# Kernel tuning notes

Hardware: AMD Instinct MI355X
Metric: run time of the kernel (lower is better)

The kernel has to match this reference:

```python
import jax, jax.numpy as jnp
import numpy as np


def conv2d(x, w, pad):
    # x: [N,C,H,W], w: [O,I,kh,kw]
    return jax.lax.conv_general_dilated(
        x, w, window_strides=(1, 1), padding=[(pad, pad), (pad, pad)],
        dimension_numbers=("NCHW", "OIHW", "NCHW"))


def group_norm1(x, g, b, eps=1e-5):
    # GroupNorm(1, C): normalize over (C,H,W) per sample, per-channel affine
    mu = jnp.mean(x, axis=(1, 2, 3), keepdims=True)
    var = jnp.mean((x - mu) ** 2, axis=(1, 2, 3), keepdims=True)
    xn = (x - mu) * jax.lax.rsqrt(var + eps)
    return xn * g[None, :, None, None] + b[None, :, None, None]


def maxpool_3x3_s2(x):
    return jax.lax.reduce_window(
        x, -jnp.inf, jax.lax.max, (1, 1, 3, 3), (1, 1, 2, 2),
        ((0, 0), (0, 0), (1, 1), (1, 1)))


def hr2o_layer(x, wq, wk, wv, wo, g, b):
    # x: [N,C,H,W]; pairwise attention over the N ROIs at each (h,w)
    q = conv2d(x, wq, 1)
    k = conv2d(x, wk, 1)
    v = conv2d(x, wv, 1)
    scale = 1.0 / jnp.sqrt(jnp.asarray(x.shape[1], x.dtype))
    # torch: (q.unsqueeze(1) * k.unsqueeze(0)).sum(2) == einsum over channels
    att = jnp.einsum("nchw,mchw->nmhw", q, k) * scale  # [N,N,H,W]
    att = jax.nn.softmax(att, axis=1)                    # softmax over keys (dim=1)
    virt = jnp.einsum("nmhw,mchw->nchw", att, v)        # [N,C,H,W]
    virt = jax.nn.relu(group_norm1(virt, g, b))
    virt = conv2d(virt, wo, 1)
    return x + virt  # dropout is identity in eval mode


def setup_inputs() -> dict:
    key = jax.random.key(0)
    ks = jax.random.split(key, 12)
    N, C_R, H, W, HID, NCLS, DEPTH = 64, 1024, 16, 16, 512, 60, 2
    s = 0.02
    return {
        "bg_feats": jax.random.normal(ks[0], (C_R, H, W), jnp.float32),
        "actor_feats": jax.random.normal(ks[1], (N, C_R), jnp.float32),
        "w_conv1": jax.random.normal(ks[2], (HID, 2 * C_R, 1, 1), jnp.float32) * s,
        "w_conv2": jax.random.normal(ks[3], (HID, HID, 3, 3), jnp.float32) * s,
        "w_q": jax.random.normal(ks[4], (DEPTH, HID, HID, 3, 3), jnp.float32) * s,
        "w_k": jax.random.normal(ks[5], (DEPTH, HID, HID, 3, 3), jnp.float32) * s,
        "w_v": jax.random.normal(ks[6], (DEPTH, HID, HID, 3, 3), jnp.float32) * s,
        "w_o": jax.random.normal(ks[7], (DEPTH, HID, HID, 3, 3), jnp.float32) * s,
        "gamma": jnp.ones((DEPTH, HID), jnp.float32),
        "beta": jnp.zeros((DEPTH, HID), jnp.float32),
        "w_fc1": jax.random.normal(ks[8], (HID, C_R), jnp.float32) * s,
        "w_fc2": jax.random.normal(ks[9], (NCLS, 2 * HID), jnp.float32) * s,
    }


def reference(bg_feats, actor_feats, w_conv1, w_conv2, w_q, w_k, w_v, w_o,
              gamma, beta, w_fc1, w_fc2):
    N = actor_feats.shape[0]
    C_R, H, W = bg_feats.shape
    # bg repeated per ROI, actor features tiled over spatial dims
    bg = jnp.broadcast_to(bg_feats[None], (N, C_R, H, W))
    tiled = jnp.broadcast_to(actor_feats[:, :, None, None], (N, C_R, H, W))
    x = jnp.concatenate([bg, tiled], axis=1)           # [N, 2*C_R, H, W]
    x = jax.nn.relu(conv2d(x, w_conv1, 0))             # 1x1 -> [N,HID,H,W]
    x = jax.nn.relu(conv2d(x, w_conv2, 0))             # 3x3 pad=0 -> H-2,W-2
    x = maxpool_3x3_s2(x)                              # -> 7x7
    for d in range(w_q.shape[0]):
        x = hr2o_layer(x, w_q[d], w_k[d], w_v[d], w_o[d], gamma[d], beta[d])
    high_order = jnp.mean(x, axis=(2, 3))              # gap -> [N,HID]
    roi = jax.nn.relu(actor_feats @ w_fc1.T)           # [N,HID]
    out = jnp.concatenate([roi, high_order], axis=1) @ w_fc2.T  # [N,num_classes]
    return out
```

## Files before the change

### kernel.cpp

```cpp
#include <hip/hip_runtime.h>
#include <math.h>


typedef __bf16 bf16x8 __attribute__((ext_vector_type(8)));
typedef float  f32x4  __attribute__((ext_vector_type(4)));

#define NROI 64
#define CR   1024
#define HIDC 512
#define NCLS 60
#define PLANE (NROI * HIDC * 49)
#define ROWH 40
#define OCALL 4608
#define TAPSTR ((size_t)OCALL * 512)
#define WL (HIDC * HIDC * 9)
#define GNCNT 25088.0f

#if defined(__has_builtin)
#  if __has_builtin(__builtin_amdgcn_global_load_lds)
#    define HAVE_GLL 1
#  endif
#endif

__device__ __forceinline__ void stage16(const void* g, void* lds_base, int lane) {
#ifdef HAVE_GLL
    __builtin_amdgcn_global_load_lds(
        (const __attribute__((address_space(1))) unsigned int*)g,
        (__attribute__((address_space(3))) unsigned int*)lds_base, 16, 0, 0);
#else
    *(uint4*)((char*)lds_base + lane * 16) = *(const uint4*)g;
#endif
}

__device__ __forceinline__ float bf2f(unsigned short h) {
    union { unsigned u; float f; } x; x.u = (unsigned)h << 16; return x.f;
}

__global__ __launch_bounds__(256) void k_misc(
    const float* __restrict__ w2, const float* __restrict__ wq,
    const float* __restrict__ wk, const float* __restrict__ wv,
    const float* __restrict__ wo, const float* __restrict__ bg,
    __bf16* __restrict__ wAll, __bf16* __restrict__ inT7,
    __bf16* __restrict__ bgT)
{
    const int b = blockIdx.x, tid = threadIdx.x;
    if (b < 4608) {
        const int bid = b;
        const float* src;
        if (bid < 512) src = w2 + (size_t)bid * 4608;
        else if (bid < 2048) {
            const int r = bid - 512;
            const float* bb = r < 512 ? wq : (r < 1024 ? wk : wv);
            src = bb + (size_t)(r & 511) * 4608;
        } else if (bid < 2560) src = wo + (size_t)(bid - 2048) * 4608;
        else if (bid < 4096) {
            const int r = bid - 2560;
            const float* bb = r < 512 ? wq : (r < 1024 ? wk : wv);
            src = bb + WL + (size_t)(r & 511) * 4608;
        } else src = wo + WL + (size_t)(bid - 4096) * 4608;
        __shared__ float s[4608];
        const float4* s4 = (const float4*)src;
        for (int i = tid; i < 1152; i += 256) ((float4*)s)[i] = s4[i];
        __syncthreads();
        unsigned* dst = (unsigned*)wAll;
        const int c = tid * 2;
        const int swz = ((c >> 3) & 3) ^ ((bid >> 1) & 3);
        const size_t cidx = (size_t)(c >> 5) * 32 + swz * 8 + (c & 7);
#pragma unroll
        for (int t = 0; t < 9; ++t) {
            const unsigned short u0 = __builtin_bit_cast(unsigned short, (__bf16)s[c * 9 + t]);
            const unsigned short u1 = __builtin_bit_cast(unsigned short, (__bf16)s[(c + 1) * 9 + t]);
            dst[((size_t)t * TAPSTR + (size_t)bid * 512 + cidx) / 2] =
                ((unsigned)u1 << 16) | u0;
        }
    } else if (b < 5120) {
        const int k = b - 4608;
        const int n = k >> 3;
        const int j0 = (k & 7) * 4;
#pragma unroll
        for (int i = 0; i < 4; ++i) {
            const int jj = j0 + i;
            int sp;
            if (jj < 9) sp = jj;
            else if (jj < 18) sp = 63 + jj;
            else { const int t = jj - 18; sp = (1 + (t >> 1)) * 9 + (t & 1) * 8; }
            unsigned* d = (unsigned*)(inT7 + ((size_t)n * 81 + sp) * 512);
            d[tid] = 0u;
        }
    } else {
        const int cb = (b - 5120) * 8;
        const int p = tid;
        bf16x8 v;
#pragma unroll
        for (int j = 0; j < 8; ++j)
            v[j] = (__bf16)bg[(size_t)(cb + j) * 256 + p];
        *(bf16x8*)(bgT + (size_t)p * 1024 + cb) = v;
    }
}

__global__ __launch_bounds__(256, 2) void k_ab(
    const __bf16* __restrict__ bgT, const float* __restrict__ actor,
    const float* __restrict__ w1, const float* __restrict__ wfc1,
    float* __restrict__ A_T, float* __restrict__ Bp, float* __restrict__ roi)
{
    const int bx = blockIdx.x, by = blockIdx.y;
    const bool isA = bx < 4;
    const bool isRoi = (bx == 5);
    const int ocWg = by * 64;
    const int tid = threadIdx.x;
    const int w = tid >> 6, lane = tid & 63;
    const int q = lane >> 4, l16 = lane & 15;

    __shared__ __align__(16) __bf16 s_a[64 * ROWH];
    __shared__ __align__(16) __bf16 s_b[64 * ROWH];

    f32x4 acc[4];
#pragma unroll
    for (int nt = 0; nt < 4; ++nt) acc[nt] = (f32x4){0.f, 0.f, 0.f, 0.f};

    const int row = tid >> 2, part = tid & 3;
    for (int ch = 0; ch < 32; ++ch) {
        const int c0 = ch * 32;
        __syncthreads();
        if (isA) {
            const uint4 vv = *(const uint4*)(
                bgT + (size_t)(bx * 64 + row) * 1024 + c0 + part * 8);
            *(uint4*)(&s_a[row * ROWH + part * 8]) = vv;
        } else {
            const float* src = actor + (size_t)row * CR + c0 + part * 8;
            bf16x8 val;
#pragma unroll
            for (int j = 0; j < 8; ++j) val[j] = (__bf16)src[j];
            *(bf16x8*)(&s_a[row * ROWH + part * 8]) = val;
        }
        {
            const float* srcb = isRoi
                ? (wfc1 + (size_t)(ocWg + row) * CR + c0 + part * 8)
                : (w1 + (size_t)(ocWg + row) * (2 * CR)
                      + (isA ? 0 : CR) + c0 + part * 8);
            bf16x8 vb;
#pragma unroll
            for (int j = 0; j < 8; ++j) vb[j] = (__bf16)srcb[j];
            *(bf16x8*)(&s_b[row * ROWH + part * 8]) = vb;
        }
        __syncthreads();
        const bf16x8 af = *(const bf16x8*)(&s_a[(w * 16 + l16) * ROWH + q * 8]);
#pragma unroll
        for (int nt = 0; nt < 4; ++nt) {
            const bf16x8 bw = *(const bf16x8*)(&s_b[(nt * 16 + l16) * ROWH + q * 8]);
            acc[nt] = __builtin_amdgcn_mfma_f32_16x16x32_bf16(af, bw, acc[nt], 0, 0, 0);
        }
    }
#pragma unroll
    for (int r = 0; r < 4; ++r) {
#pragma unroll
        for (int nt = 0; nt < 4; ++nt) {
            const int mrow = w * 16 + q * 4 + r;
            const int oc = ocWg + nt * 16 + l16;
            if (isA)       A_T[(size_t)(bx * 64 + mrow) * 512 + oc] = acc[nt][r];
            else if (isRoi) roi[(size_t)mrow * 512 + oc] = fmaxf(acc[nt][r], 0.f);
            else           Bp[(size_t)mrow * 512 + oc] = acc[nt][r];
        }
    }
}

__global__ __launch_bounds__(256) void k_prep_in2(
    const float* __restrict__ A_T, const float* __restrict__ B,
    __bf16* __restrict__ dst)
{
    const int vn = blockIdx.x;
    const int n = vn >> 2, quad = vn & 3;
    const int sp0 = blockIdx.y * 27;
    const float b0 = B[n * HIDC + threadIdx.x];
    const float b1 = B[n * HIDC + 256 + threadIdx.x];
    for (int sp = sp0; sp < sp0 + 27; ++sp) {
        const int r = sp / 9, w = sp % 9;
        const int p16 = ((quad >> 1) * 7 + r) * 16 + (quad & 1) * 7 + w;
        __bf16* d = dst + ((size_t)vn * 81 + sp) * 512;
        d[threadIdx.x]       = (__bf16)fmaxf(A_T[p16 * HIDC + threadIdx.x] + b0, 0.f);
        d[256 + threadIdx.x] = (__bf16)fmaxf(A_T[p16 * HIDC + 256 + threadIdx.x] + b1, 0.f);
    }
}

__global__ __launch_bounds__(256) void k_prep_gn(
    const float* __restrict__ virt, const float* __restrict__ statsRaw,
    const float* __restrict__ gamma, const float* __restrict__ beta,
    __bf16* __restrict__ gnT)
{
    const int vn = blockIdx.x;
    const int sp0 = blockIdx.y * 9;
    __shared__ float s_mi[2];
    if (threadIdx.x == 0) {
        const float S = statsRaw[vn * 2], Q = statsRaw[vn * 2 + 1];
        const float mean = S / GNCNT;
        s_mi[0] = mean;
        s_mi[1] = rsqrtf(Q / GNCNT - mean * mean + 1e-5f);
    }
    __syncthreads();
    const float m = s_mi[0], iv = s_mi[1];
    const int c0 = threadIdx.x, c1 = threadIdx.x + 256;
    const float g0 = gamma[c0], g1 = gamma[c1];
    const float b0 = beta[c0],  b1 = beta[c1];
    for (int sp = sp0; sp < sp0 + 9; ++sp) {
        const int rr = sp / 9, cc = sp % 9;
        __bf16* d = gnT + ((size_t)vn * 81 + sp) * 512;
        if (rr >= 1 && rr <= 7 && cc >= 1 && cc <= 7) {
            const int p = (rr - 1) * 7 + (cc - 1);
            const float* src = virt + ((size_t)vn * 49 + p) * 512;
            d[c0] = (__bf16)fmaxf((src[c0] - m) * iv * g0 + b0, 0.f);
            d[c1] = (__bf16)fmaxf((src[c1] - m) * iv * g1 + b1, 0.f);
        } else {
            d[c0] = (__bf16)0.f;
            d[c1] = (__bf16)0.f;
        }
    }
}

template<int VN, int MODE>
__global__ __launch_bounds__(256, (VN == 4) ? 2 : 3) void k_conv_pipe(
    const __bf16* __restrict__ inT,
    const __bf16* __restrict__ wAll, int ocBaseGl,
    __bf16* __restrict__ outb,
    float* __restrict__ zeroStats, float* __restrict__ gapZero,
    const float* __restrict__ resid, float* __restrict__ outf,
    __bf16* __restrict__ inT7out, float* __restrict__ gapOut)
{
    constexpr int MT = (VN == 4) ? 4 : 2;
    constexpr int SLOTS = VN * 324;
    constexpr int NSUB = (SLOTS + 255) / 256;
    constexpr int SBUF = NSUB * 256;
    constexpr int NI = NSUB / 3;
    const int tid = threadIdx.x;
    const int w = tid >> 6, lane = tid & 63;
    const int q = lane >> 4, l16 = lane & 15;
    const int vn_l = (VN == 4) ? w : (w & 1);
    const int mh   = (VN == 4) ? 0 : (w >> 1);
    const int vnBase = blockIdx.x * VN;
    const int ocWg = blockIdx.y * 64;

    if (zeroStats && blockIdx.x == 0 && blockIdx.y == 0 && tid < 128)
        zeroStats[tid] = 0.f;
    if (gapZero && blockIdx.y == 0 && blockIdx.x < 16) {
        const float4 z = {0.f, 0.f, 0.f, 0.f};
        ((float4*)gapZero)[blockIdx.x * 512 + tid * 2]     = z;
        ((float4*)gapZero)[blockIdx.x * 512 + tid * 2 + 1] = z;
    }

    __shared__ __align__(16) __bf16 s_w[2 * 3 * 2048];
    __shared__ __align__(16) __bf16 s_in[2 * SBUF * 8];

    unsigned iGo[NSUB];
#pragma unroll
    for (int s = 0; s < NSUB; ++s) {
        int idx = tid + s * 256;
        if (idx > SLOTS - 1) idx = SLOTS - 1;
        const int vnl = idx / 324, rem = idx - vnl * 324;
        const int r = rem >> 2, part = rem & 3;
        iGo[s] = (unsigned)(((vnBase + vnl) * 81 + r) * 512
                            + ((part ^ (r & 3)) * 8));
    }
    const unsigned wGo = (unsigned)((ocBaseGl + ocWg + (tid >> 2)) * 512
                                    + (tid & 3) * 8);
    const int bOff = l16 * 32 + ((q ^ ((l16 >> 1) & 3)) << 3);

    int aLoc[MT];
#pragma unroll
    for (int mt = 0; mt < MT; ++mt) {
        int p = (mh * MT + mt) * 16 + l16;
        p = p > 48 ? 48 : p;
        aLoc[mt] = (p / 7) * 9 + (p % 7);
    }
    const int vb81 = vn_l * 81;

    f32x4 acc[MT][4];
#pragma unroll
    for (int a = 0; a < MT; ++a)
#pragma unroll
        for (int b = 0; b < 4; ++b) acc[a][b] = (f32x4){0.f, 0.f, 0.f, 0.f};

#pragma unroll
    for (int s = 0; s < NSUB; ++s)
        stage16(inT + iGo[s],
                (char*)s_in + (size_t)(s * 256 + w * 64) * 16, lane);
#pragma unroll
    for (int j = 0; j < 3; ++j)
        stage16(wAll + (size_t)j * TAPSTR + wGo,
                (char*)s_w + (size_t)j * 4096 + (size_t)w * 1024, lane);
    __syncthreads();

    for (int ch = 0; ch < 16; ++ch) {
        const int c0 = ch * 32;
        const int cur = ch & 1;
        const int nxt = cur ^ 1;
#pragma unroll
        for (int f = 0; f < 3; ++f) {
            const int P = ch * 3 + f;
            const int wpar = P & 1;
            {
                const int fn = (f == 2) ? 0 : (f + 1);
                const int cc = (f == 2) ? (c0 + 32) : c0;
#pragma unroll
                for (int j = 0; j < 3; ++j)
                    stage16(wAll + (size_t)(fn * 3 + j) * TAPSTR + wGo + cc,
                            (char*)s_w + (size_t)((wpar ^ 1) * 3 + j) * 4096
                                        + (size_t)w * 1024, lane);
            }
#pragma unroll
            for (int u = 0; u < NI; ++u) {
                const int s = f * NI + u;
                stage16(inT + iGo[s] + c0 + 32,
                        (char*)s_in + (size_t)nxt * (SBUF * 16)
                                    + (size_t)(s * 256 + w * 64) * 16, lane);
            }
            if (f == 0) {
                if constexpr (NI == 2) asm volatile("s_waitcnt vmcnt(5)" ::: "memory");
                else                   asm volatile("s_waitcnt vmcnt(4)" ::: "memory");
            } else {
                if constexpr (NI == 2) asm volatile("s_waitcnt vmcnt(7)" ::: "memory");
                else                   asm volatile("s_waitcnt vmcnt(5)" ::: "memory");
            }
            __builtin_amdgcn_sched_barrier(0);
            __builtin_amdgcn_s_barrier();
            __builtin_amdgcn_sched_barrier(0);
            __builtin_amdgcn_s_setprio(1);
#pragma unroll
            for (int j = 0; j < 3; ++j) {
                const int DT = f * 9 + j;
                bf16x8 bw[4];
#pragma unroll
                for (int nt = 0; nt < 4; ++nt)
                    bw[nt] = *(const bf16x8*)(
                        &s_w[(wpar * 3 + j) * 2048 + nt * 512 + bOff]);
                bf16x8 af[MT];
#pragma unroll
                for (int mt = 0; mt < MT; ++mt) {
                    const int rl = aLoc[mt] + DT;
                    const int col = (q ^ (rl & 3)) << 3;
                    af[mt] = *(const bf16x8*)(
                        &s_in[cur * (SBUF * 8) + (vb81 + rl) * 32 + col]);
                }
#pragma unroll
                for (int mt = 0; mt < MT; ++mt)
#pragma unroll
                    for (int nt = 0; nt < 4; ++nt)
                        acc[mt][nt] = __builtin_amdgcn_mfma_f32_16x16x32_bf16(
                            af[mt], bw[nt], acc[mt][nt], 0, 0, 0);
            }
            __builtin_amdgcn_s_setprio(0);
            __builtin_amdgcn_sched_barrier(0);
            __builtin_amdgcn_s_barrier();
        }
    }

    const int vn = vnBase + vn_l;
    float gsum[4] = {0.f, 0.f, 0.f, 0.f};
#pragma unroll
    for (int mt = 0; mt < MT; ++mt) {
#pragma unroll
        for (int r = 0; r < 4; ++r) {
            const int p = (mh * MT + mt) * 16 + q * 4 + r;
            if (p >= 49) continue;
#pragma unroll
            for (int nt = 0; nt < 4; ++nt) {
                const int oc = ocWg + nt * 16 + l16;
                const float v = acc[mt][nt][r];
                if constexpr (MODE == 2) {
                    const int n = vn >> 2, quad = vn & 3;
                    const int p14 = ((quad >> 1) * 7 + p / 7) * 14 + (quad & 1) * 7 + p % 7;
                    outb[((size_t)n * 196 + p14) * 512 + oc] = (__bf16)fmaxf(v, 0.f);
                } else if constexpr (MODE == 1) {
                    const size_t addr = ((size_t)vn * 49 + p) * 512 + oc;
                    const float res = v + resid[addr];
                    if (!gapOut) outf[addr] = res;
                    gsum[nt] += res;
                    if (inT7out) {
                        const int sp = (p / 7 + 1) * 9 + (p % 7 + 1);
                        inT7out[((size_t)vn * 81 + sp) * 512 + oc] = (__bf16)res;
                    }
                } else {
                    const int conv = oc >> 9;
                    outb[(size_t)conv * PLANE + ((size_t)p * 64 + vn) * 512 + (oc & 511)]
                        = (__bf16)v;
                }
            }
        }
    }
    if constexpr (MODE == 1) {
        if (gapOut) {
#pragma unroll
            for (int nt = 0; nt < 4; ++nt)
                atomicAdd(gapOut + (size_t)vn * 512 + ocWg + nt * 16 + l16, gsum[nt]);
        }
    }
}

__global__ __launch_bounds__(256) void k_pool_prep(
    const __bf16* __restrict__ x2, __bf16* __restrict__ inT7,
    float* __restrict__ xA)
{
    const int b = blockIdx.x;
    const int n = b / 49, p = b % 49;
    const int i = p / 7, j = p % 7;
    const int sp = (i + 1) * 9 + (j + 1);
#pragma unroll
    for (int k = 0; k < 2; ++k) {
        const int c = threadIdx.x + k * 256;
        float mx = -1e30f;
#pragma unroll
        for (int di = -1; di <= 1; ++di) {
            const int rr = 2 * i + di;
            if (rr < 0 || rr >= 14) continue;
#pragma unroll
            for (int dj = -1; dj <= 1; ++dj) {
                const int cc = 2 * j + dj;
                if (cc < 0 || cc >= 14) continue;
                mx = fmaxf(mx, (float)x2[((size_t)n * 196 + rr * 14 + cc) * 512 + c]);
            }
        }
        inT7[((size_t)n * 81 + sp) * 512 + c] = (__bf16)mx;
        xA[((size_t)n * 49 + p) * 512 + c] = mx;
    }
}

__global__ __launch_bounds__(256) void k_attvirt(
    const __bf16* __restrict__ qT, const __bf16* __restrict__ kT,
    const __bf16* __restrict__ vT, float* __restrict__ virt,
    float* __restrict__ statsRaw)
{
    const int p = blockIdx.y;
    const int w = threadIdx.x >> 6, m = threadIdx.x & 63;
    const int n = blockIdx.x * 4 + w;
    __shared__ float s_q[4][HIDC];
    __shared__ float s_a[4][64];
    {
        const uint4 v = ((const uint4*)(qT + ((size_t)p * 64 + n) * HIDC))[m];
        const unsigned* u = (const unsigned*)&v;
#pragma unroll
        for (int j = 0; j < 4; ++j) {
            s_q[w][m * 8 + 2 * j]     = bf2f((unsigned short)(u[j] & 0xffff));
            s_q[w][m * 8 + 2 * j + 1] = bf2f((unsigned short)(u[j] >> 16));
        }
    }
    __syncthreads();
    const uint4* krow = (const uint4*)(kT + ((size_t)p * 64 + m) * HIDC);
    float acc0 = 0.f, acc1 = 0.f;
    for (int i = 0; i < 64; ++i) {
        const uint4 v = krow[i];
        const unsigned* u = (const unsigned*)&v;
#pragma unroll
        for (int j = 0; j < 2; ++j) {
            acc0 = fmaf(s_q[w][i * 8 + 2 * j],     bf2f((unsigned short)(u[j] & 0xffff)), acc0);
            acc0 = fmaf(s_q[w][i * 8 + 2 * j + 1], bf2f((unsigned short)(u[j] >> 16)),    acc0);
        }
#pragma unroll
        for (int j = 2; j < 4; ++j) {
            acc1 = fmaf(s_q[w][i * 8 + 2 * j],     bf2f((unsigned short)(u[j] & 0xffff)), acc1);
            acc1 = fmaf(s_q[w][i * 8 + 2 * j + 1], bf2f((unsigned short)(u[j] >> 16)),    acc1);
        }
    }
    float acc = (acc0 + acc1) * 0.044194173824159216f;
    float mx = acc;
#pragma unroll
    for (int off = 32; off; off >>= 1) mx = fmaxf(mx, __shfl_xor(mx, off));
    const float e = expf(acc - mx);
    float s = e;
#pragma unroll
    for (int off = 32; off; off >>= 1) s += __shfl_xor(s, off);
    s_a[w][m] = e / s;
    __syncthreads();
    const int c0 = m * 8;
    float av[8];
#pragma unroll
    for (int j = 0; j < 8; ++j) av[j] = 0.f;
    for (int mm = 0; mm < 64; ++mm) {
        const float a = s_a[w][mm];
        const uint4 v = *(const uint4*)(vT + ((size_t)p * 64 + mm) * HIDC + c0);
        const unsigned* u = (const unsigned*)&v;
#pragma unroll
        for (int j = 0; j < 4; ++j) {
            av[2 * j]     = fmaf(a, bf2f((unsigned short)(u[j] & 0xffff)), av[2 * j]);
            av[2 * j + 1] = fmaf(a, bf2f((unsigned short)(u[j] >> 16)),    av[2 * j + 1]);
        }
    }
    float* o = virt + ((size_t)n * 49 + p) * 512 + c0;
    float ps = 0.f, pq = 0.f;
#pragma unroll
    for (int j = 0; j < 8; ++j) {
        o[j] = av[j];
        ps += av[j];
        pq = fmaf(av[j], av[j], pq);
    }
#pragma unroll
    for (int off = 32; off; off >>= 1) {
        ps += __shfl_xor(ps, off);
        pq += __shfl_xor(pq, off);
    }
    if (m == 0) {
        atomicAdd(statsRaw + n * 2, ps);
        atomicAdd(statsRaw + n * 2 + 1, pq);
    }
}

__global__ __launch_bounds__(256) void k_final(
    const float* __restrict__ roi, const float* __restrict__ gap,
    const float* __restrict__ wfc2, float* __restrict__ out)
{
    const int n = blockIdx.x, tid = threadIdx.x;
    __shared__ float s[1024];
    s[tid]       = roi[(size_t)n * 512 + tid];
    s[tid + 256] = roi[(size_t)n * 512 + 256 + tid];
    s[tid + 512] = gap[(size_t)n * 512 + tid] * (1.f / 49.f);
    s[tid + 768] = gap[(size_t)n * 512 + 256 + tid] * (1.f / 49.f);
    __syncthreads();
    if (tid < 240) {
        const int k = tid >> 2, part = tid & 3;
        const float4* w4 = (const float4*)(wfc2 + (size_t)k * 1024 + part * 256);
        const float4* s4 = (const float4*)(s + part * 256);
        float a0 = 0.f, a1 = 0.f, a2 = 0.f, a3 = 0.f;
        for (int i = 0; i < 64; ++i) {
            const float4 wv = w4[i], sv = s4[i];
            a0 = fmaf(wv.x, sv.x, a0); a1 = fmaf(wv.y, sv.y, a1);
            a2 = fmaf(wv.z, sv.z, a2); a3 = fmaf(wv.w, sv.w, a3);
        }
        float acc = (a0 + a1) + (a2 + a3);
        acc += __shfl_xor(acc, 1);
        acc += __shfl_xor(acc, 2);
        if (part == 0) out[n * NCLS + k] = acc;
    }
}

extern "C" void kernel_launch(void* const* d_in, const int* in_sizes, int n_in,
                              void* d_out, int out_size, void* d_ws, size_t ws_size,
                              hipStream_t stream) {
    const float* bg    = (const float*)d_in[0];
    const float* actor = (const float*)d_in[1];
    const float* w1    = (const float*)d_in[2];
    const float* w2    = (const float*)d_in[3];
    const float* wq    = (const float*)d_in[4];
    const float* wk    = (const float*)d_in[5];
    const float* wv    = (const float*)d_in[6];
    const float* wo    = (const float*)d_in[7];
    const float* gamma = (const float*)d_in[8];
    const float* beta  = (const float*)d_in[9];
    const float* wfc1  = (const float*)d_in[10];
    const float* wfc2  = (const float*)d_in[11];
    float* out = (float*)d_out;
    float* ws  = (float*)d_ws;

    float* A_T   = ws;
    float* Bp    = A_T + 131072;
    float* xA    = Bp + 32768;
    float* xB    = xA + PLANE;
    float* stats = xB + PLANE;
    float* roi   = stats + 128;
    float* gap   = roi + 32768;
    float* fend  = gap + 32768;
    __bf16* x2h  = (__bf16*)fend;
    float*  virt = (float*)x2h;
    __bf16* inT2 = x2h + 6422528;
    __bf16* qkvT = inT2;
    __bf16* inT7 = inT2 + 10616832;
    __bf16* wAll = inT7 + 2654208;
    __bf16* bgT  = wAll + (size_t)9 * OCALL * 512;
    __bf16* gnT  = bgT + 262144;

    k_misc<<<5248, 256, 0, stream>>>(w2, wq, wk, wv, wo, bg, wAll, inT7, bgT);
    k_ab<<<dim3(6, 8), 256, 0, stream>>>(bgT, actor, w1, wfc1, A_T, Bp, roi);
    k_prep_in2<<<dim3(256, 3), 256, 0, stream>>>(A_T, Bp, inT2);
    k_conv_pipe<4, 2><<<dim3(64, 8), 256, 0, stream>>>(
        inT2, wAll, 0, x2h, nullptr, nullptr,
        nullptr, nullptr, nullptr, nullptr);
    k_pool_prep<<<64 * 49, 256, 0, stream>>>(x2h, inT7, xA);

    float* xin = xA;
    float* xout = xB;
    for (int d = 0; d < 2; ++d) {
        k_conv_pipe<2, 0><<<dim3(32, 24), 256, 0, stream>>>(
            inT7, wAll, 512 + d * 2048, qkvT, stats,
            d == 1 ? gap : nullptr,
            nullptr, nullptr, nullptr, nullptr);
        k_attvirt<<<dim3(16, 49), 256, 0, stream>>>(
            qkvT, qkvT + PLANE, qkvT + 2 * PLANE, virt, stats);
        k_prep_gn<<<dim3(64, 9), 256, 0, stream>>>(
            virt, stats, gamma + d * HIDC, beta + d * HIDC, gnT);
        k_conv_pipe<2, 1><<<dim3(32, 8), 256, 0, stream>>>(
            gnT, wAll, 2048 + d * 2048, nullptr, nullptr, nullptr,
            xin, xout, d == 0 ? inT7 : nullptr, d == 1 ? gap : nullptr);
        float* t = xin; xin = xout; xout = t;
    }
    k_final<<<64, 256, 0, stream>>>(roi, gap, wfc2, out);
}
```

Measured before the change: 593.8 us.

## Fuse GroupNorm prep into output conv prologue and vectorize attention LDS reads

Removes the separate k_prep_gn launch. Each output-conv block now normalizes, applies ReLU and writes its own ROIs' 7x7 interior into the padded bf16 buffer, then syncs before the conv main loop. The zero border of gnT is written once in k_misc instead of on every layer. The attention kernel also switches to float4 LDS reads for q and the softmax weights. The fused prologue is recomputed by all 8 oc-blocks per ROI pair, and the conv reads gnT via global loads that may race with other blocks' writes to neighbouring ROIs, so correctness depends on each block reading only its own ROIs.

```diff
diff --git a/kernel.cpp b/kernel.cpp
--- a/kernel.cpp
+++ b/kernel.cpp
@@ -41,7 +41,7 @@
     const float* __restrict__ wk, const float* __restrict__ wv,
     const float* __restrict__ wo, const float* __restrict__ bg,
     __bf16* __restrict__ wAll, __bf16* __restrict__ inT7,
-    __bf16* __restrict__ bgT)
+    __bf16* __restrict__ bgT, __bf16* __restrict__ gnT)
 {
     const int b = blockIdx.x, tid = threadIdx.x;
     if (b < 4608) {
@@ -73,8 +73,9 @@
             dst[((size_t)t * TAPSTR + (size_t)bid * 512 + cidx) / 2] =
                 ((unsigned)u1 << 16) | u0;
         }
-    } else if (b < 5120) {
-        const int k = b - 4608;
+    } else if (b < 5120 || b >= 5248) {
+        const int k = (b < 5120) ? (b - 4608) : (b - 5248);
+        __bf16* base = (b < 5120) ? inT7 : gnT;
         const int n = k >> 3;
         const int j0 = (k & 7) * 4;
 #pragma unroll
@@ -84,7 +85,7 @@
             if (jj < 9) sp = jj;
             else if (jj < 18) sp = 63 + jj;
             else { const int t = jj - 18; sp = (1 + (t >> 1)) * 9 + (t & 1) * 8; }
-            unsigned* d = (unsigned*)(inT7 + ((size_t)n * 81 + sp) * 512);
+            unsigned* d = (unsigned*)(base + ((size_t)n * 81 + sp) * 512);
             d[tid] = 0u;
         }
     } else {
@@ -182,40 +183,6 @@
     }
 }
 
-__global__ __launch_bounds__(256) void k_prep_gn(
-    const float* __restrict__ virt, const float* __restrict__ statsRaw,
-    const float* __restrict__ gamma, const float* __restrict__ beta,
-    __bf16* __restrict__ gnT)
-{
-    const int vn = blockIdx.x;
-    const int sp0 = blockIdx.y * 9;
-    __shared__ float s_mi[2];
-    if (threadIdx.x == 0) {
-        const float S = statsRaw[vn * 2], Q = statsRaw[vn * 2 + 1];
-        const float mean = S / GNCNT;
-        s_mi[0] = mean;
-        s_mi[1] = rsqrtf(Q / GNCNT - mean * mean + 1e-5f);
-    }
-    __syncthreads();
-    const float m = s_mi[0], iv = s_mi[1];
-    const int c0 = threadIdx.x, c1 = threadIdx.x + 256;
-    const float g0 = gamma[c0], g1 = gamma[c1];
-    const float b0 = beta[c0],  b1 = beta[c1];
-    for (int sp = sp0; sp < sp0 + 9; ++sp) {
-        const int rr = sp / 9, cc = sp % 9;
-        __bf16* d = gnT + ((size_t)vn * 81 + sp) * 512;
-        if (rr >= 1 && rr <= 7 && cc >= 1 && cc <= 7) {
-            const int p = (rr - 1) * 7 + (cc - 1);
-            const float* src = virt + ((size_t)vn * 49 + p) * 512;
-            d[c0] = (__bf16)fmaxf((src[c0] - m) * iv * g0 + b0, 0.f);
-            d[c1] = (__bf16)fmaxf((src[c1] - m) * iv * g1 + b1, 0.f);
-        } else {
-            d[c0] = (__bf16)0.f;
-            d[c1] = (__bf16)0.f;
-        }
-    }
-}
-
 template<int VN, int MODE>
 __global__ __launch_bounds__(256, (VN == 4) ? 2 : 3) void k_conv_pipe(
     const __bf16* __restrict__ inT,
@@ -223,7 +190,10 @@
     __bf16* __restrict__ outb,
     float* __restrict__ zeroStats, float* __restrict__ gapZero,
     const float* __restrict__ resid, float* __restrict__ outf,
-    __bf16* __restrict__ inT7out, float* __restrict__ gapOut)
+    __bf16* __restrict__ inT7out, float* __restrict__ gapOut,
+    const float* __restrict__ vin, const float* __restrict__ statsRaw,
+    const float* __restrict__ gnG, const float* __restrict__ gnB,
+    __bf16* __restrict__ gnTout)
 {
     constexpr int MT = (VN == 4) ? 4 : 2;
     constexpr int SLOTS = VN * 324;
@@ -244,6 +214,35 @@
         const float4 z = {0.f, 0.f, 0.f, 0.f};
         ((float4*)gapZero)[blockIdx.x * 512 + tid * 2]     = z;
         ((float4*)gapZero)[blockIdx.x * 512 + tid * 2 + 1] = z;
+    }
+
+    if constexpr (MODE == 1) {
+        const int vh = tid >> 7;
+        const int vnn = vnBase + vh;
+        const float S = statsRaw[vnn * 2], Q = statsRaw[vnn * 2 + 1];
+        const float mean = S / GNCNT;
+        const float iv = rsqrtf(Q / GNCNT - mean * mean + 1e-5f);
+        const int t128 = tid & 127;
+        for (int ck = t128; ck < 3136; ck += 128) {
+            const int p = ck >> 6, c8 = (ck & 63) * 8;
+            const float* src = vin + ((size_t)vnn * 49 + p) * 512 + c8;
+            const f32x4 a = *(const f32x4*)(src);
+            const f32x4 bq = *(const f32x4*)(src + 4);
+            const f32x4 g0 = *(const f32x4*)(gnG + c8);
+            const f32x4 g1 = *(const f32x4*)(gnG + c8 + 4);
+            const f32x4 b0 = *(const f32x4*)(gnB + c8);
+            const f32x4 b1 = *(const f32x4*)(gnB + c8 + 4);
+            bf16x8 val;
+#pragma unroll
+            for (int j = 0; j < 4; ++j)
+                val[j] = (__bf16)fmaxf((a[j] - mean) * iv * g0[j] + b0[j], 0.f);
+#pragma unroll
+            for (int j = 0; j < 4; ++j)
+                val[4 + j] = (__bf16)fmaxf((bq[j] - mean) * iv * g1[j] + b1[j], 0.f);
+            const int sp = (p / 7 + 1) * 9 + (p % 7 + 1);
+            *(bf16x8*)(gnTout + ((size_t)vnn * 81 + sp) * 512 + c8) = val;
+        }
+        __syncthreads();
     }
 
     __shared__ __align__(16) __bf16 s_w[2 * 3 * 2048];
@@ -430,8 +429,8 @@
     const int p = blockIdx.y;
     const int w = threadIdx.x >> 6, m = threadIdx.x & 63;
     const int n = blockIdx.x * 4 + w;
-    __shared__ float s_q[4][HIDC];
-    __shared__ float s_a[4][64];
+    __shared__ __align__(16) float s_q[4][HIDC];
+    __shared__ __align__(16) float s_a[4][64];
     {
         const uint4 v = ((const uint4*)(qT + ((size_t)p * 64 + n) * HIDC))[m];
         const unsigned* u = (const unsigned*)&v;
@@ -447,16 +446,16 @@
     for (int i = 0; i < 64; ++i) {
         const uint4 v = krow[i];
         const unsigned* u = (const unsigned*)&v;
-#pragma unroll
-        for (int j = 0; j < 2; ++j) {
-            acc0 = fmaf(s_q[w][i * 8 + 2 * j],     bf2f((unsigned short)(u[j] & 0xffff)), acc0);
-            acc0 = fmaf(s_q[w][i * 8 + 2 * j + 1], bf2f((unsigned short)(u[j] >> 16)),    acc0);
-        }
-#pragma unroll
-        for (int j = 2; j < 4; ++j) {
-            acc1 = fmaf(s_q[w][i * 8 + 2 * j],     bf2f((unsigned short)(u[j] & 0xffff)), acc1);
-            acc1 = fmaf(s_q[w][i * 8 + 2 * j + 1], bf2f((unsigned short)(u[j] >> 16)),    acc1);
-        }
+        const float4 qa = *(const float4*)(&s_q[w][i * 8]);
+        const float4 qb = *(const float4*)(&s_q[w][i * 8 + 4]);
+        acc0 = fmaf(qa.x, bf2f((unsigned short)(u[0] & 0xffff)), acc0);
+        acc0 = fmaf(qa.y, bf2f((unsigned short)(u[0] >> 16)),    acc0);
+        acc0 = fmaf(qa.z, bf2f((unsigned short)(u[1] & 0xffff)), acc0);
+        acc0 = fmaf(qa.w, bf2f((unsigned short)(u[1] >> 16)),    acc0);
+        acc1 = fmaf(qb.x, bf2f((unsigned short)(u[2] & 0xffff)), acc1);
+        acc1 = fmaf(qb.y, bf2f((unsigned short)(u[2] >> 16)),    acc1);
+        acc1 = fmaf(qb.z, bf2f((unsigned short)(u[3] & 0xffff)), acc1);
+        acc1 = fmaf(qb.w, bf2f((unsigned short)(u[3] >> 16)),    acc1);
     }
     float acc = (acc0 + acc1) * 0.044194173824159216f;
     float mx = acc;
@@ -472,14 +471,18 @@
     float av[8];
 #pragma unroll
     for (int j = 0; j < 8; ++j) av[j] = 0.f;
-    for (int mm = 0; mm < 64; ++mm) {
-        const float a = s_a[w][mm];
-        const uint4 v = *(const uint4*)(vT + ((size_t)p * 64 + mm) * HIDC + c0);
-        const unsigned* u = (const unsigned*)&v;
-#pragma unroll
-        for (int j = 0; j < 4; ++j) {
-            av[2 * j]     = fmaf(a, bf2f((unsigned short)(u[j] & 0xffff)), av[2 * j]);
-            av[2 * j + 1] = fmaf(a, bf2f((unsigned short)(u[j] >> 16)),    av[2 * j + 1]);
+    for (int mm = 0; mm < 64; mm += 4) {
+        const float4 a4 = *(const float4*)(&s_a[w][mm]);
+#pragma unroll
+        for (int k = 0; k < 4; ++k) {
+            const float a = ((const float*)&a4)[k];
+            const uint4 v = *(const uint4*)(vT + ((size_t)p * 64 + mm + k) * HIDC + c0);
+            const unsigned* u = (const unsigned*)&v;
+#pragma unroll
+            for (int j = 0; j < 4; ++j) {
+                av[2 * j]     = fmaf(a, bf2f((unsigned short)(u[j] & 0xffff)), av[2 * j]);
+                av[2 * j + 1] = fmaf(a, bf2f((unsigned short)(u[j] >> 16)),    av[2 * j + 1]);
+            }
         }
     }
     float* o = virt + ((size_t)n * 49 + p) * 512 + c0;
@@ -564,12 +567,13 @@
     __bf16* bgT  = wAll + (size_t)9 * OCALL * 512;
     __bf16* gnT  = bgT + 262144;
 
-    k_misc<<<5248, 256, 0, stream>>>(w2, wq, wk, wv, wo, bg, wAll, inT7, bgT);
+    k_misc<<<5760, 256, 0, stream>>>(w2, wq, wk, wv, wo, bg, wAll, inT7, bgT, gnT);
     k_ab<<<dim3(6, 8), 256, 0, stream>>>(bgT, actor, w1, wfc1, A_T, Bp, roi);
     k_prep_in2<<<dim3(256, 3), 256, 0, stream>>>(A_T, Bp, inT2);
     k_conv_pipe<4, 2><<<dim3(64, 8), 256, 0, stream>>>(
         inT2, wAll, 0, x2h, nullptr, nullptr,
-        nullptr, nullptr, nullptr, nullptr);
+        nullptr, nullptr, nullptr, nullptr,
+        nullptr, nullptr, nullptr, nullptr, nullptr);
     k_pool_prep<<<64 * 49, 256, 0, stream>>>(x2h, inT7, xA);
 
     float* xin = xA;
@@ -578,14 +582,14 @@
         k_conv_pipe<2, 0><<<dim3(32, 24), 256, 0, stream>>>(
             inT7, wAll, 512 + d * 2048, qkvT, stats,
             d == 1 ? gap : nullptr,
-            nullptr, nullptr, nullptr, nullptr);
+            nullptr, nullptr, nullptr, nullptr,
+            nullptr, nullptr, nullptr, nullptr, nullptr);
         k_attvirt<<<dim3(16, 49), 256, 0, stream>>>(
             qkvT, qkvT + PLANE, qkvT + 2 * PLANE, virt, stats);
-        k_prep_gn<<<dim3(64, 9), 256, 0, stream>>>(
-            virt, stats, gamma + d * HIDC, beta + d * HIDC, gnT);
         k_conv_pipe<2, 1><<<dim3(32, 8), 256, 0, stream>>>(
             gnT, wAll, 2048 + d * 2048, nullptr, nullptr, nullptr,
-            xin, xout, d == 0 ? inT7 : nullptr, d == 1 ? gap : nullptr);
+            xin, xout, d == 0 ? inT7 : nullptr, d == 1 ? gap : nullptr,
+            virt, stats, gamma + d * HIDC, beta + d * HIDC, gnT);
         float* t = xin; xin = xout; xout = t;
     }
     k_final<<<64, 256, 0, stream>>>(roi, gap, wfc2, out);
```

Result: slower. 613.2 us (+3.3%).
